# Kernel optimization log

Hardware: AMD Instinct MI355X
Metric: run time of the kernel (lower is better)

## Reference

```python
import jax, jax.numpy as jnp
import numpy as np

B, W, G, E, NI, K = 2048, 8192, 8, 128, 16, 15


def setup_inputs() -> dict:
    key = jax.random.key(0)
    ks = jax.random.split(key, 12)
    wavelengths_nm = jnp.linspace(300.0, 400.0, W, dtype=jnp.float32)
    # Rayleigh optical depth (Hansen & Travis style approximation), AMF=1 column
    lam_um = wavelengths_nm / 1000.0
    rayleigh_od = (0.008569 * lam_um ** -4
                   * (1.0 + 0.0113 * lam_um ** -2 + 0.00013 * lam_um ** -4)).astype(jnp.float32)
    return {
        "gas_columns": jax.random.uniform(ks[0], (B, G), jnp.float32),
        "instrument_ids": jax.random.randint(ks[1], (B,), 0, NI),
        "nuisance_latent": jax.random.normal(ks[2], (B, G), jnp.float32),
        "air_mass": 1.0 + 2.0 * jax.random.uniform(ks[3], (B,), jnp.float32),
        "wavelengths_nm": wavelengths_nm,
        "absorption": 0.1 * jax.random.uniform(ks[4], (G, W), jnp.float32),
        "continuum_basis": 0.05 * jax.random.normal(ks[5], (G + 1, W), jnp.float32),
        "rayleigh_od": rayleigh_od,
        "embed_table": jax.random.normal(ks[6], (NI, E), jnp.float32),
        "w1": jax.random.normal(ks[7], (E + G, 64), jnp.float32) / np.sqrt(E + G),
        "b1": jnp.zeros((64,), jnp.float32),
        "w2": jax.random.normal(ks[8], (64, 7), jnp.float32) / 8.0,
        "b2": jnp.zeros((7,), jnp.float32),
    }


def _gaussian_kernel(width_px, kernel_size):
    half = (kernel_size - 1) / 2
    pos = jnp.linspace(-half, half, kernel_size, dtype=width_px.dtype)  # [K]
    k = jnp.exp(-0.5 * (pos[None, :] / (width_px[:, None] + 1e-6)) ** 2)  # [B,K]
    return k / k.sum(axis=1, keepdims=True)


def _forward(gas_columns, nuisance_latent, air_mass, wavelengths_nm, absorption,
             continuum_basis, rayleigh_od, embed_table, w1, b1, w2, b2,
             instrument_ids):
    b = gas_columns.shape[0]
    am = air_mass[:, None]                                   # [B,1]
    scaled = gas_columns * am                                # [B,G]
    optical_depth = scaled @ absorption                      # [B,W]
    ones = jnp.ones((b, 1), gas_columns.dtype)
    continuum = jnp.concatenate([gas_columns, ones], axis=1) @ continuum_basis  # [B,W]
    differential = optical_depth + continuum + am * rayleigh_od[None, :]

    # nuisance MLP on [latent, embedding]
    embed = embed_table[instrument_ids]                      # [B,E]
    nin = jnp.concatenate([nuisance_latent, embed], axis=-1)
    h = jax.nn.gelu(nin @ w1 + b1, approximate=False)
    p = h @ w2 + b2                                          # [B,7]

    gain = jax.nn.softplus(p[:, 0]) + 0.001
    offset = p[:, 1]
    woff = 0.05 * jnp.tanh(p[:, 2])
    wscale = 1.0 + 0.005 * jnp.tanh(p[:, 3])
    lsf = jnp.clip(jax.nn.softplus(p[:, 4]) + 0.001, 0.2, 5.0)
    stray = jax.nn.sigmoid(p[:, 5]) * 0.05
    nonlin = 0.02 * jnp.tanh(p[:, 6])

    # per-sample wavelength shift/scale + linear resampling
    new_wl = wavelengths_nm[None, :] * wscale[:, None] + woff[:, None]  # [B,W]
    differential = jax.vmap(lambda wq, d: jnp.interp(wq, wavelengths_nm, d))(new_wl, differential)

    # per-sample Gaussian LSF convolution (replicate padding)
    kernel = _gaussian_kernel(lsf, K)                        # [B,K]
    pad = K // 2
    padded = jnp.pad(differential, ((0, 0), (pad, pad)), mode='edge')  # [B,W+K-1]
    n = differential.shape[1]
    convolved = sum(padded[:, k:k + n] * kernel[:, k:k + 1] for k in range(K))

    counts = jnp.exp(-convolved)
    post = gain[:, None] * counts + offset[:, None]
    total_nl = jnp.clip(nonlin, -0.04, 0.04)                 # instrument nonlinearity = 0
    nl_counts = post + total_nl[:, None] * post ** 2
    total_stray = jnp.clip(stray, 0.0, 0.2)                  # instrument stray = 0
    simulated = (1.0 - total_stray[:, None]) * nl_counts \
        + total_stray[:, None] * nl_counts.mean(axis=1, keepdims=True)
    return simulated


def reference(gas_columns, instrument_ids, nuisance_latent, air_mass,
              wavelengths_nm, absorption, continuum_basis, rayleigh_od,
              embed_table, w1, b1, w2, b2):
    return _forward(gas_columns, nuisance_latent, air_mass, wavelengths_nm,
                    absorption, continuum_basis, rayleigh_od, embed_table,
                    w1, b1, w2, b2, instrument_ids)
```

## Files before the change

### kernel.cpp

```cpp
#include <hip/hip_runtime.h>

#define W_ 8192
#define NBATCH 2048
#define NT 256
#define NWAVE 4
#define SEGW 2048
#define CCH 256
#define NCHW 8
#define IRW 272

typedef unsigned short u16_t;
typedef _Float16 h2v __attribute__((ext_vector_type(2)));

__device__ __forceinline__ u16_t f2h(float x){ _Float16 h=(_Float16)x; return __builtin_bit_cast(u16_t,h); }
__device__ __forceinline__ float h2f(u16_t u){ return (float)__builtin_bit_cast(_Float16,u); }
__device__ __forceinline__ unsigned pk2(float a,float b){ return (unsigned)f2h(a)|((unsigned)f2h(b)<<16); }
__device__ __forceinline__ float dot2u(unsigned a,unsigned b,float c){
#if __has_builtin(__builtin_amdgcn_fdot2)
  return __builtin_amdgcn_fdot2(__builtin_bit_cast(h2v,a),__builtin_bit_cast(h2v,b),c,false);
#else
  h2v ha=__builtin_bit_cast(h2v,a), hb=__builtin_bit_cast(h2v,b);
  return c+(float)ha[0]*(float)hb[0]+(float)ha[1]*(float)hb[1];
#endif
}
__device__ __forceinline__ unsigned pkrtz(float a,float b){
#if __has_builtin(__builtin_amdgcn_cvt_pkrtz)
  return __builtin_bit_cast(unsigned, __builtin_amdgcn_cvt_pkrtz(a,b));
#else
  return pk2(a,b);
#endif
}
__device__ __forceinline__ unsigned alignb(unsigned hi, unsigned lo){
#if __has_builtin(__builtin_amdgcn_alignbit)
  return __builtin_amdgcn_alignbit(hi, lo, 16);
#else
  return (lo >> 16) | (hi << 16);
#endif
}
__device__ __forceinline__ float softplusf(float x){ return fmaxf(x,0.f)+log1pf(expf(-fabsf(x))); }
__device__ __forceinline__ unsigned rflv(unsigned v){
  return (unsigned)__builtin_amdgcn_readfirstlane((int)v);
}
__device__ __forceinline__ float rflvf(float v){
  return __builtin_bit_cast(float, __builtin_amdgcn_readfirstlane(__builtin_bit_cast(int, v)));
}

__global__ __launch_bounds__(256, 2)
void doas_prep(const float* __restrict__ absn, const float* __restrict__ cbn,
               const float* __restrict__ ray, const int* __restrict__ iid,
               const float* __restrict__ nuis, const float* __restrict__ emb,
               const float* __restrict__ w1, const float* __restrict__ b1,
               const float* __restrict__ w2, const float* __restrict__ b2,
               unsigned* __restrict__ Tp, float* __restrict__ params){
  const int tid = threadIdx.x;
  const int b = blockIdx.x;
  __shared__ float hS[4][64];
  __shared__ float pS[4][8];

  if (b < 32){
    const int w = b*256 + tid;
    #pragma unroll
    for (int q=0;q<4;++q) Tp[q*W_+w]     = pk2(absn[(2*q)*W_+w], absn[(2*q+1)*W_+w]);
    #pragma unroll
    for (int q=0;q<4;++q) Tp[(4+q)*W_+w] = pk2(cbn[(2*q)*W_+w],  cbn[(2*q+1)*W_+w]);
    Tp[8*W_+w] = pk2(cbn[8*W_+w], ray[w]);
  }

  {
    const int rl = tid >> 6, j = tid & 63;
    const int r = b*4 + rl;
    const int id = iid[r];
    float acc = b1[j];
    const float* nrow = nuis + (size_t)r * 8;
    #pragma unroll
    for (int i = 0; i < 8; ++i) acc = fmaf(nrow[i], w1[i*64 + j], acc);
    const float* erow = emb + (size_t)id * 128;
    for (int i = 0; i < 128; ++i) acc = fmaf(erow[i], w1[(8+i)*64 + j], acc);
    hS[rl][j] = 0.5f * acc * (1.0f + erff(acc * 0.70710678118654752f));
  }
  __syncthreads();
  if (tid < 4*7){
    const int rl = tid / 7, k = tid % 7;
    float p = b2[k];
    for (int j = 0; j < 64; ++j) p = fmaf(hS[rl][j], w2[j*7+k], p);
    pS[rl][k] = p;
  }
  __syncthreads();
  if (tid < 4){
    const int rl = tid;
    const int r = b*4 + rl;
    float p0=pS[rl][0], p1=pS[rl][1], p2=pS[rl][2], p3=pS[rl][3],
          p4=pS[rl][4], p5=pS[rl][5], p6=pS[rl][6];
    float gainv = softplusf(p0) + 0.001f;
    float offv  = p1;
    float woffv = 0.05f * tanhf(p2);
    float wscv  = 1.0f + 0.005f * tanhf(p3);
    float lsf   = fminf(fmaxf(softplusf(p4) + 0.001f, 0.2f), 5.0f);
    float strv  = fminf(fmaxf((1.0f/(1.0f+expf(-p5))) * 0.05f, 0.0f), 0.2f);
    float nlin  = fminf(fmaxf(0.02f * tanhf(p6), -0.04f), 0.04f);
    float iw = 1.0f/(lsf + 1e-6f);
    float ks[15]; float ksum = 0.f;
    #pragma unroll
    for (int k2=0;k2<15;++k2){ float pp=(float)(k2-7)*iw; float e=expf(-0.5f*pp*pp); ks[k2]=e; ksum+=e; }
    float inv = 1.0f/ksum;
    float* pr = params + (size_t)r*16;
    unsigned* pu = (unsigned*)pr;
    #pragma unroll
    for (int i=0;i<7;++i) pu[i] = pk2(ks[2*i]*inv, ks[2*i+1]*inv);
    pu[7] = pk2(ks[14]*inv, 0.0f);
    pr[9]  = wscv;
    pr[10] = (300.0f*(wscv - 1.0f) + woffv) * (8191.0f/100.0f);
    pr[11] = gainv; pr[12] = offv; pr[13] = nlin; pr[14] = strv;
    pr[15] = 0.f;
  }
}

template<bool CLO, bool CHI>
__device__ __forceinline__ void interp_chunk(int cbase, int l, const unsigned* __restrict__ rU,
                                             unsigned* __restrict__ irowU,
                                             float wscale, float posoff){
  #pragma unroll
  for (int it=0; it<3; ++it){
    const int pi = it*64 + l;
    if (pi < 136){
      float v2[2];
      #pragma unroll
      for (int u=0;u<2;++u){
        int j = cbase + 2*pi + u;
        if (CLO) j = max(j, 0);
        if (CHI) j = min(j, W_-1);
        float pos = fmaf((float)j, wscale, posoff);
        if (CLO) pos = fmaxf(pos, 0.0f);
        if (CHI) pos = fminf(pos, 8191.0f);
        int i0 = (int)pos;
        if (CHI) i0 = min(i0, W_-2);
        const float fr = pos - (float)i0;
        const int m = i0 >> 1;
        const unsigned u0 = rU[m];
        const unsigned u1 = rU[m+1];
        const unsigned hu0 = u0 >> 16;
        const bool odd = (i0 & 1);
        const unsigned ua = odd ? hu0 : u0;
        const unsigned ub = odd ? u1  : hu0;
        const float d0 = h2f((u16_t)ua);
        const float d1 = h2f((u16_t)ub);
        v2[u] = fmaf(fr, d1-d0, d0);
      }
      irowU[pi] = pkrtz(v2[0], v2[1]);
    }
  }
}

__global__ __launch_bounds__(NT, 2)
void doas_main7(const unsigned* __restrict__ Tp, const float* __restrict__ gas,
                const float* __restrict__ air, const float* __restrict__ params,
                float* __restrict__ out){
  __shared__ u16_t rowH[W_ + 16];
  __shared__ u16_t irowS[NWAVE][IRW];
  __shared__ float wsumS[NWAVE];

  const int tid = threadIdx.x;
  const int row = blockIdx.x;
  const int wid = tid >> 6, l = tid & 63;
  const int segbase = wid * SEGW;

  unsigned csg[9];
  {
    const float am = air[row];
    const float* gfp = gas + (size_t)row * 8;
    #pragma unroll
    for (int q=0;q<4;++q) csg[q]   = rflv(pk2(gfp[2*q]*am, gfp[2*q+1]*am));
    #pragma unroll
    for (int q=0;q<4;++q) csg[4+q] = rflv(pk2(gfp[2*q],    gfp[2*q+1]));
    csg[8] = rflv(pk2(1.0f, am));
  }

  const float* pr = params + (size_t)row * 16;
  const unsigned* pu = (const unsigned*)pr;
  unsigned kwp[7];
  #pragma unroll
  for (int i=0;i<7;++i) kwp[i] = rflv(pu[i]);
  const unsigned k14lo = rflv(pu[7]);
  const float wscale = rflvf(pr[9]),  posoff = rflvf(pr[10]);
  const float gainv  = rflvf(pr[11]), offv   = rflvf(pr[12]);
  const float nlin   = rflvf(pr[13]), strv   = rflvf(pr[14]);

  unsigned* rowHU = (unsigned*)rowH;
  #pragma unroll
  for (int it=0; it<8; ++it){
    const int e0 = it*1024 + tid*4;
    uint4 dq[9];
    #pragma unroll
    for (int q=0;q<9;++q) dq[q] = *(const uint4*)(Tp + q*W_ + e0);
    float a0=0.f, a1=0.f, a2=0.f, a3=0.f;
    #pragma unroll
    for (int q=0;q<9;++q){
      a0 = dot2u(dq[q].x, csg[q], a0);
      a1 = dot2u(dq[q].y, csg[q], a1);
      a2 = dot2u(dq[q].z, csg[q], a2);
      a3 = dot2u(dq[q].w, csg[q], a3);
    }
    *(uint2*)(rowHU + (e0 >> 1)) = make_uint2(pkrtz(a0,a1), pkrtz(a2,a3));
  }
  __syncthreads();

  const unsigned* rU = (const unsigned*)rowH;
  u16_t* irow = &irowS[wid][0];
  unsigned* irowU = (unsigned*)irow;

  float accsum = 0.f;
  unsigned nlp[NCHW][2];

  #pragma unroll
  for (int c = 0; c < NCHW; ++c) {
    const int cs = segbase + c*CCH;
    const int cbase = cs - 8;
    if (wid == 0 && c == 0)
      interp_chunk<true,false>(cbase, l, rU, irowU, wscale, posoff);
    else if (wid == NWAVE-1 && c == NCHW-1)
      interp_chunk<false,true>(cbase, l, rU, irowU, wscale, posoff);
    else
      interp_chunk<false,false>(cbase, l, rU, irowU, wscale, posoff);
    __builtin_amdgcn_wave_barrier();
    {
      const uint2* p2 = (const uint2*)irowU + l;
      const uint2 A = p2[0], B = p2[1], C = p2[2], D = p2[3], E = p2[4];
      unsigned q[10] = {A.x,A.y, B.x,B.y, C.x,C.y, D.x,D.y, E.x,E.y};
      unsigned sh[9];
      #pragma unroll
      for (int m=0;m<9;++m) sh[m] = alignb(q[m+1], q[m]);
      float nlv[4];
      #pragma unroll
      for (int t=0;t<4;++t){
        float cv = 0.f;
        if ((t & 1) == 0){
          const int b0 = t >> 1;
          #pragma unroll
          for (int i=0;i<7;++i) cv = dot2u(sh[b0+i], kwp[i], cv);
          cv = dot2u(sh[b0+7], k14lo, cv);
        } else {
          const int b0 = (t+1) >> 1;
          #pragma unroll
          for (int i=0;i<7;++i) cv = dot2u(q[b0+i], kwp[i], cv);
          cv = dot2u(q[b0+7], k14lo, cv);
        }
        const float counts = __expf(-cv);
        const float post = fmaf(gainv, counts, offv);
        const float v = fmaf(nlin*post, post, post);
        accsum += v;
        nlv[t] = v;
      }
      nlp[c][0] = pkrtz(nlv[0], nlv[1]);
      nlp[c][1] = pkrtz(nlv[2], nlv[3]);
    }
    __builtin_amdgcn_wave_barrier();
  }

  float s = accsum;
  #pragma unroll
  for (int off2 = 32; off2 >= 1; off2 >>= 1) s += __shfl_down(s, off2);
  if (l == 0) wsumS[wid] = s;
  __syncthreads();
  const float meanv = (wsumS[0]+wsumS[1]+wsumS[2]+wsumS[3]) * (1.0f/8192.0f);

  {
    const float aa = 1.0f - strv;
    const float bb = strv * meanv;
    float* orow = out + (size_t)row * W_;
    #pragma unroll
    for (int c = 0; c < NCHW; ++c) {
      const unsigned u0 = nlp[c][0], u1 = nlp[c][1];
      float4 o0;
      o0.x = fmaf(aa, h2f((u16_t)(u0 & 0xffffu)), bb);
      o0.y = fmaf(aa, h2f((u16_t)(u0 >> 16)),     bb);
      o0.z = fmaf(aa, h2f((u16_t)(u1 & 0xffffu)), bb);
      o0.w = fmaf(aa, h2f((u16_t)(u1 >> 16)),     bb);
      *(float4*)(orow + segbase + c*CCH + 4*l) = o0;
    }
  }
}

__global__ __launch_bounds__(256, 2)
void doas_mono(const float* __restrict__ gas, const int* __restrict__ iid,
               const float* __restrict__ nuis, const float* __restrict__ air,
               const float* __restrict__ absn, const float* __restrict__ cbn,
               const float* __restrict__ ray, const float* __restrict__ emb,
               const float* __restrict__ w1, const float* __restrict__ b1,
               const float* __restrict__ w2, const float* __restrict__ b2,
               float* __restrict__ out)
{
  __shared__ u16_t ringS[4][2048];
  __shared__ u16_t irowS2[4][544];
  __shared__ float hS[64];
  __shared__ float pS[8];
  __shared__ float scalS[52];
  __shared__ float wsumS[4];

  const int tid = threadIdx.x;
  const int row = blockIdx.x;

  if (tid < 64) {
    const int j = tid;
    const int id = iid[row];
    float acc = b1[j];
    const float* nrow = nuis + (size_t)row * 8;
    #pragma unroll
    for (int i = 0; i < 8; ++i) acc = fmaf(nrow[i], w1[i*64 + j], acc);
    const float* erow = emb + (size_t)id * 128;
    for (int i = 0; i < 128; ++i) acc = fmaf(erow[i], w1[(8+i)*64 + j], acc);
    hS[j] = 0.5f * acc * (1.0f + erff(acc * 0.70710678118654752f));
  }
  __syncthreads();
  if (tid < 7) {
    float p = b2[tid];
    for (int j = 0; j < 64; ++j) p = fmaf(hS[j], w2[j*7+tid], p);
    pS[tid] = p;
  }
  __syncthreads();
  if (tid == 0) {
    float p0=pS[0], p1=pS[1], p2=pS[2], p3=pS[3], p4=pS[4], p5=pS[5], p6=pS[6];
    float gainv = softplusf(p0) + 0.001f;
    float offv  = p1;
    float woffv = 0.05f * tanhf(p2);
    float wscv  = 1.0f + 0.005f * tanhf(p3);
    float lsf   = fminf(fmaxf(softplusf(p4) + 0.001f, 0.2f), 5.0f);
    float strv  = fminf(fmaxf((1.0f/(1.0f+expf(-p5))) * 0.05f, 0.0f), 0.2f);
    float nlin  = fminf(fmaxf(0.02f * tanhf(p6), -0.04f), 0.04f);
    float iw = 1.0f/(lsf + 1e-6f);
    float ks[15]; float ksum = 0.f;
    #pragma unroll
    for (int k2=0;k2<15;++k2){ float pp=(float)(k2-7)*iw; float e=expf(-0.5f*pp*pp); ks[k2]=e; ksum+=e; }
    float inv = 1.0f/ksum;
    scalS[15] = wscv;
    scalS[16] = (300.0f*(wscv - 1.0f) + woffv) * (8191.0f/100.0f);
    scalS[17] = gainv; scalS[18] = offv; scalS[19] = nlin; scalS[20] = strv;
    scalS[22] = air[row];
    unsigned* su = (unsigned*)scalS;
    #pragma unroll
    for (int i=0;i<7;++i) su[32+i] = pk2(ks[2*i]*inv, ks[2*i+1]*inv);
    su[39] = pk2(ks[14]*inv, 0.0f);
    su[40] = pk2(0.0f, ks[14]*inv);
    #pragma unroll
    for (int g=0; g<8; ++g) scalS[23+g] = gas[(size_t)row*8+g];
  }
  __syncthreads();

  const int wid = tid >> 6, l = tid & 63;
  const int segbase = wid * 2048;
  const unsigned* scalU = (const unsigned*)scalS;
  unsigned kwp[7];
  #pragma unroll
  for (int i=0;i<7;++i) kwp[i] = rflv(scalU[32+i]);
  const unsigned k14lo = rflv(scalU[39]), k14hi = rflv(scalU[40]);
  const float wscale = scalS[15], posoff = scalS[16];
  const float gainv  = scalS[17], offv   = scalS[18];
  const float nlin   = scalS[19], strv   = scalS[20];

  u16_t* ring = &ringS[wid][0];
  unsigned* ringU = (unsigned*)ring;
  u16_t* irow = &irowS2[wid][0];
  unsigned* irowU = (unsigned*)irow;

  auto do_diff = [&](int s){
    const int sbase = segbase - 256 + (s << 9);
    #pragma unroll
    for (int it=0; it<4; ++it){
      const int e0 = sbase + ((it*64 + l) << 1);
      const int eL = min(max(e0, 0), W_-2);
      const float am = scalS[22];
      float a0=0.f, a1=0.f;
      #pragma unroll
      for (int g=0; g<8; ++g){
        const float cg = scalS[23+g];
        const float ca = cg*am;
        a0 = fmaf(ca, absn[g*W_+eL],   a0); a0 = fmaf(cg, cbn[g*W_+eL],   a0);
        a1 = fmaf(ca, absn[g*W_+eL+1], a1); a1 = fmaf(cg, cbn[g*W_+eL+1], a1);
      }
      a0 += cbn[8*W_+eL]   + am*ray[eL];
      a1 += cbn[8*W_+eL+1] + am*ray[eL+1];
      ringU[((unsigned)e0 & 2047) >> 1] = pkrtz(a0, a1);
    }
  };

  float accsum = 0.f;
  unsigned nlp[4][4];

  do_diff(0); do_diff(1);
  __builtin_amdgcn_wave_barrier();

  #pragma unroll
  for (int c = 0; c < 4; ++c) {
    if (c < 3) do_diff(c+2);
    __builtin_amdgcn_wave_barrier();
    {
      const int cbase = segbase + (c << 9) - 8;
      #pragma unroll
      for (int it = 0; it < 5; ++it) {
        const int pi = it*64 + l;
        if (pi < 264) {
          float v2[2];
          #pragma unroll
          for (int u=0; u<2; ++u){
            const int j = cbase + 2*pi + u;
            const int jc = min(max(j, 0), W_-1);
            float pos = fmaf((float)jc, wscale, posoff);
            pos = fminf(fmaxf(pos, 0.0f), 8191.0f);
            const int i0 = min((int)pos, W_-2);
            const float fr = pos - (float)i0;
            const float d0 = h2f(ring[ i0    & 2047]);
            const float d1 = h2f(ring[(i0+1) & 2047]);
            v2[u] = fmaf(fr, d1-d0, d0);
          }
          irowU[pi] = pkrtz(v2[0], v2[1]);
        }
      }
    }
    __builtin_amdgcn_wave_barrier();
    {
      const uint4* qp = (const uint4*)irow + l;
      const uint4 A = qp[0], B = qp[1], C = qp[2];
      unsigned q[12] = {A.x,A.y,A.z,A.w, B.x,B.y,B.z,B.w, C.x,C.y,C.z,C.w};
      unsigned sh[10];
      #pragma unroll
      for (int m=0;m<10;++m) sh[m] = alignb(q[m+1], q[m]);
      float nlv[8];
      #pragma unroll
      for (int t=0;t<8;++t){
        const int s2 = t >> 1;
        float cv = 0.f;
        if ((t & 1) == 0){
          #pragma unroll
          for (int i=0;i<7;++i) cv = dot2u(sh[s2+i], kwp[i], cv);
          cv = dot2u(q[s2+7], k14hi, cv);
        } else {
          #pragma unroll
          for (int i=0;i<7;++i) cv = dot2u(q[s2+1+i], kwp[i], cv);
          cv = dot2u(q[s2+8], k14lo, cv);
        }
        const float counts = __expf(-cv);
        const float post = fmaf(gainv, counts, offv);
        const float v = fmaf(nlin*post, post, post);
        accsum += v;
        nlv[t] = v;
      }
      nlp[c][0] = pkrtz(nlv[0], nlv[1]);
      nlp[c][1] = pkrtz(nlv[2], nlv[3]);
      nlp[c][2] = pkrtz(nlv[4], nlv[5]);
      nlp[c][3] = pkrtz(nlv[6], nlv[7]);
    }
    __builtin_amdgcn_wave_barrier();
  }

  float s = accsum;
  #pragma unroll
  for (int off2 = 32; off2 >= 1; off2 >>= 1) s += __shfl_down(s, off2);
  if (l == 0) wsumS[wid] = s;
  __syncthreads();
  const float meanv = (wsumS[0]+wsumS[1]+wsumS[2]+wsumS[3]) * (1.0f/8192.0f);

  {
    const float aa = 1.0f - strv;
    const float bb = strv * meanv;
    float* orow = out + (size_t)row * W_;
    #pragma unroll
    for (int c = 0; c < 4; ++c) {
      const unsigned u0 = nlp[c][0], u1 = nlp[c][1], u2 = nlp[c][2], u3 = nlp[c][3];
      float4 o0, o1;
      o0.x = fmaf(aa, h2f((u16_t)(u0 & 0xffffu)), bb);
      o0.y = fmaf(aa, h2f((u16_t)(u0 >> 16)),     bb);
      o0.z = fmaf(aa, h2f((u16_t)(u1 & 0xffffu)), bb);
      o0.w = fmaf(aa, h2f((u16_t)(u1 >> 16)),     bb);
      o1.x = fmaf(aa, h2f((u16_t)(u2 & 0xffffu)), bb);
      o1.y = fmaf(aa, h2f((u16_t)(u2 >> 16)),     bb);
      o1.z = fmaf(aa, h2f((u16_t)(u3 & 0xffffu)), bb);
      o1.w = fmaf(aa, h2f((u16_t)(u3 >> 16)),     bb);
      float* dst = orow + segbase + (c << 9) + 8*l;
      *(float4*)(dst)     = o0;
      *(float4*)(dst + 4) = o1;
    }
  }
}

extern "C" void kernel_launch(void* const* d_in, const int* in_sizes, int n_in,
                              void* d_out, int out_size, void* d_ws, size_t ws_size,
                              hipStream_t stream) {
  const float* gas  = (const float*)d_in[0];
  const int*   iid  = (const int*)d_in[1];
  const float* nuis = (const float*)d_in[2];
  const float* air  = (const float*)d_in[3];
  const float* wl   = (const float*)d_in[4];
  const float* absn = (const float*)d_in[5];
  const float* cbn  = (const float*)d_in[6];
  const float* ray  = (const float*)d_in[7];
  const float* emb  = (const float*)d_in[8];
  const float* w1   = (const float*)d_in[9];
  const float* b1   = (const float*)d_in[10];
  const float* w2   = (const float*)d_in[11];
  const float* b2   = (const float*)d_in[12];
  float* out = (float*)d_out;
  (void)in_sizes; (void)n_in; (void)out_size; (void)wl;

  const size_t packBytes = (size_t)9 * W_ * 4;
  const size_t parBytes  = (size_t)NBATCH * 16 * 4;

  if (ws_size >= packBytes + parBytes) {
    unsigned* Tp  = (unsigned*)d_ws;
    float* params = (float*)((char*)d_ws + packBytes);
    hipLaunchKernelGGL(doas_prep, dim3(NBATCH/4), dim3(256), 0, stream,
                       absn, cbn, ray, iid, nuis, emb, w1, b1, w2, b2, Tp, params);
    hipLaunchKernelGGL(doas_main7, dim3(NBATCH), dim3(NT), 0, stream,
                       Tp, gas, air, params, out);
  } else {
    hipLaunchKernelGGL(doas_mono, dim3(NBATCH), dim3(256), 0, stream,
                       gas, iid, nuis, air, absn, cbn, ray, emb, w1, b1, w2, b2, out);
  }
}
```

Before: 51.62 us.

## Restructure prep kernel: 16 rows per block, wave-shuffle second MLP layer

Result: slower. 71.94 us (+39.4%).

```diff
diff --git a/kernel.cpp b/kernel.cpp
--- a/kernel.cpp
+++ b/kernel.cpp
@@ -46,72 +46,78 @@
 }
 
 __global__ __launch_bounds__(256, 2)
-void doas_prep(const float* __restrict__ absn, const float* __restrict__ cbn,
-               const float* __restrict__ ray, const int* __restrict__ iid,
-               const float* __restrict__ nuis, const float* __restrict__ emb,
-               const float* __restrict__ w1, const float* __restrict__ b1,
-               const float* __restrict__ w2, const float* __restrict__ b2,
-               unsigned* __restrict__ Tp, float* __restrict__ params){
+void doas_prep3(const float* __restrict__ absn, const float* __restrict__ cbn,
+                const float* __restrict__ ray, const int* __restrict__ iid,
+                const float* __restrict__ nuis, const float* __restrict__ emb,
+                const float* __restrict__ w1, const float* __restrict__ b1,
+                const float* __restrict__ w2, const float* __restrict__ b2,
+                unsigned* __restrict__ Tp, float* __restrict__ params){
   const int tid = threadIdx.x;
   const int b = blockIdx.x;
-  __shared__ float hS[4][64];
-  __shared__ float pS[4][8];
-
-  if (b < 32){
-    const int w = b*256 + tid;
-    #pragma unroll
-    for (int q=0;q<4;++q) Tp[q*W_+w]     = pk2(absn[(2*q)*W_+w], absn[(2*q+1)*W_+w]);
-    #pragma unroll
-    for (int q=0;q<4;++q) Tp[(4+q)*W_+w] = pk2(cbn[(2*q)*W_+w],  cbn[(2*q+1)*W_+w]);
-    Tp[8*W_+w] = pk2(cbn[8*W_+w], ray[w]);
-  }
+  const int wid = tid >> 6, l = tid & 63;
 
   {
-    const int rl = tid >> 6, j = tid & 63;
-    const int r = b*4 + rl;
-    const int id = iid[r];
-    float acc = b1[j];
-    const float* nrow = nuis + (size_t)r * 8;
-    #pragma unroll
-    for (int i = 0; i < 8; ++i) acc = fmaf(nrow[i], w1[i*64 + j], acc);
-    const float* erow = emb + (size_t)id * 128;
-    for (int i = 0; i < 128; ++i) acc = fmaf(erow[i], w1[(8+i)*64 + j], acc);
-    hS[rl][j] = 0.5f * acc * (1.0f + erff(acc * 0.70710678118654752f));
-  }
-  __syncthreads();
-  if (tid < 4*7){
-    const int rl = tid / 7, k = tid % 7;
-    float p = b2[k];
-    for (int j = 0; j < 64; ++j) p = fmaf(hS[rl][j], w2[j*7+k], p);
-    pS[rl][k] = p;
-  }
-  __syncthreads();
-  if (tid < 4){
-    const int rl = tid;
-    const int r = b*4 + rl;
-    float p0=pS[rl][0], p1=pS[rl][1], p2=pS[rl][2], p3=pS[rl][3],
-          p4=pS[rl][4], p5=pS[rl][5], p6=pS[rl][6];
-    float gainv = softplusf(p0) + 0.001f;
-    float offv  = p1;
-    float woffv = 0.05f * tanhf(p2);
-    float wscv  = 1.0f + 0.005f * tanhf(p3);
-    float lsf   = fminf(fmaxf(softplusf(p4) + 0.001f, 0.2f), 5.0f);
-    float strv  = fminf(fmaxf((1.0f/(1.0f+expf(-p5))) * 0.05f, 0.0f), 0.2f);
-    float nlin  = fminf(fmaxf(0.02f * tanhf(p6), -0.04f), 0.04f);
-    float iw = 1.0f/(lsf + 1e-6f);
-    float ks[15]; float ksum = 0.f;
-    #pragma unroll
-    for (int k2=0;k2<15;++k2){ float pp=(float)(k2-7)*iw; float e=expf(-0.5f*pp*pp); ks[k2]=e; ksum+=e; }
-    float inv = 1.0f/ksum;
-    float* pr = params + (size_t)r*16;
-    unsigned* pu = (unsigned*)pr;
-    #pragma unroll
-    for (int i=0;i<7;++i) pu[i] = pk2(ks[2*i]*inv, ks[2*i+1]*inv);
-    pu[7] = pk2(ks[14]*inv, 0.0f);
-    pr[9]  = wscv;
-    pr[10] = (300.0f*(wscv - 1.0f) + woffv) * (8191.0f/100.0f);
-    pr[11] = gainv; pr[12] = offv; pr[13] = nlin; pr[14] = strv;
-    pr[15] = 0.f;
+    const int w = b*64 + (tid & 63);
+    if (wid == 0){
+      #pragma unroll
+      for (int q=0;q<4;++q) Tp[q*W_+w]     = pk2(absn[(2*q)*W_+w], absn[(2*q+1)*W_+w]);
+      #pragma unroll
+      for (int q=0;q<4;++q) Tp[(4+q)*W_+w] = pk2(cbn[(2*q)*W_+w],  cbn[(2*q+1)*W_+w]);
+      Tp[8*W_+w] = pk2(cbn[8*W_+w], ray[w]);
+    }
+  }
+
+  #pragma unroll
+  for (int rr = 0; rr < 4; ++rr){
+    const int r = b*16 + wid*4 + rr;
+    float hj;
+    {
+      const int id = iid[r];
+      float acc = b1[l];
+      const float* nrow = nuis + (size_t)r * 8;
+      #pragma unroll
+      for (int i = 0; i < 8; ++i) acc = fmaf(nrow[i], w1[i*64 + l], acc);
+      const float* erow = emb + (size_t)id * 128;
+      #pragma unroll 8
+      for (int i = 0; i < 128; ++i) acc = fmaf(erow[i], w1[(8+i)*64 + l], acc);
+      hj = 0.5f * acc * (1.0f + erff(acc * 0.70710678118654752f));
+    }
+    float pv[7];
+    {
+      const float* w2r = w2 + l*7;
+      #pragma unroll
+      for (int k=0;k<7;++k) pv[k] = hj * w2r[k];
+      #pragma unroll
+      for (int off=32; off>=1; off>>=1){
+        #pragma unroll
+        for (int k=0;k<7;++k) pv[k] += __shfl_down(pv[k], off);
+      }
+    }
+    if (l == 0){
+      float p0=pv[0]+b2[0], p1=pv[1]+b2[1], p2=pv[2]+b2[2], p3=pv[3]+b2[3],
+            p4=pv[4]+b2[4], p5=pv[5]+b2[5], p6=pv[6]+b2[6];
+      float gainv = softplusf(p0) + 0.001f;
+      float offv  = p1;
+      float woffv = 0.05f * tanhf(p2);
+      float wscv  = 1.0f + 0.005f * tanhf(p3);
+      float lsf   = fminf(fmaxf(softplusf(p4) + 0.001f, 0.2f), 5.0f);
+      float strv  = fminf(fmaxf((1.0f/(1.0f+expf(-p5))) * 0.05f, 0.0f), 0.2f);
+      float nlin  = fminf(fmaxf(0.02f * tanhf(p6), -0.04f), 0.04f);
+      float iw = 1.0f/(lsf + 1e-6f);
+      float ks[15]; float ksum = 0.f;
+      #pragma unroll
+      for (int k2=0;k2<15;++k2){ float pp=(float)(k2-7)*iw; float e=expf(-0.5f*pp*pp); ks[k2]=e; ksum+=e; }
+      float inv = 1.0f/ksum;
+      float* pr = params + (size_t)r*16;
+      unsigned* pu = (unsigned*)pr;
+      #pragma unroll
+      for (int i=0;i<7;++i) pu[i] = pk2(ks[2*i]*inv, ks[2*i+1]*inv);
+      pu[7] = pk2(ks[14]*inv, 0.0f);
+      pr[9]  = wscv;
+      pr[10] = (300.0f*(wscv - 1.0f) + woffv) * (8191.0f/100.0f);
+      pr[11] = gainv; pr[12] = offv; pr[13] = nlin; pr[14] = strv;
+      pr[15] = 0.f;
+    }
   }
 }
 
@@ -506,7 +512,7 @@
   if (ws_size >= packBytes + parBytes) {
     unsigned* Tp  = (unsigned*)d_ws;
     float* params = (float*)((char*)d_ws + packBytes);
-    hipLaunchKernelGGL(doas_prep, dim3(NBATCH/4), dim3(256), 0, stream,
+    hipLaunchKernelGGL(doas_prep3, dim3(NBATCH/16), dim3(256), 0, stream,
                        absn, cbn, ray, iid, nuis, emb, w1, b1, w2, b2, Tp, params);
     hipLaunchKernelGGL(doas_main7, dim3(NBATCH), dim3(NT), 0, stream,
                        Tp, gas, air, params, out);
```
